# Optimization experiments

Hardware: AMD Instinct MI355X
Metric: run time of the kernel (lower is better)

Reference implementation:

```python
import jax, jax.numpy as jnp
import numpy as np

B, S, D = 8, 4096, 1024
G, V = 2, 320
TAU = 1.0
EPS = 1e-7


def setup_inputs() -> dict:
    key = jax.random.key(0)
    k_x, k_w, k_cb, k_u = jax.random.split(key, 4)
    x = jax.random.normal(k_x, (B, S, D), dtype=jnp.float32)
    W = jax.random.normal(k_w, (D, G * V), dtype=jnp.float32) * (1.0 / np.sqrt(D))
    b = jnp.zeros((G * V,), dtype=jnp.float32)
    # nn.init.uniform_ -> U(0,1); codebooks viewed as [G, V, D//G]
    codebooks = jax.random.uniform(k_cb, (G, V, D // G), dtype=jnp.float32)
    # standard Gumbel(0,1) noise, one per logit: shape [B*S*G, V]
    u = jax.random.uniform(k_u, (B * S * G, V), dtype=jnp.float32,
                           minval=1e-6, maxval=1.0 - 1e-6)
    gumbel = -jnp.log(-jnp.log(u))
    return {"x": x, "W": W, "b": b, "codebooks": codebooks, "gumbel": gumbel}


def reference(x, W, b, codebooks, gumbel):
    Bx, Sx, Dx = x.shape
    Gx, Vx, _ = codebooks.shape
    N = Bx * Sx
    # logit projection: [B,S,D] @ [D, G*V] -> flatten to [N*G, V]
    logits = (jnp.einsum('bsd,de->bse', x, W) + b).reshape(N * Gx, Vx)
    # gumbel-softmax, hard=True with straight-through estimator
    y_soft = jax.nn.softmax((logits + gumbel) / TAU, axis=-1)
    idx = jnp.argmax(y_soft, axis=-1)
    y_hard = jax.nn.one_hot(idx, Vx, dtype=y_soft.dtype)
    one_hot_st = y_hard + y_soft - jax.lax.stop_gradient(y_soft)  # fwd == y_hard
    # codebook lookup via (mostly one-hot) contraction: [N,G,V] x [G,V,d] -> [N,G,d]
    q = jnp.einsum('ngv,gvd->ngd', one_hot_st.reshape(N, Gx, Vx), codebooks)
    quantized = q.reshape(Bx, Sx, Dx)
    # perplexity from clean (non-gumbel) softmax probs
    probs = jax.nn.softmax(logits.reshape(N, Gx, Vx), axis=-1)
    avg_probs = probs.mean(axis=0)  # [G, V]
    perplexity = jnp.exp(-jnp.sum(avg_probs * jnp.log(avg_probs + EPS), axis=-1)).mean()
    return (quantized, perplexity)
```

## Files before the change

kernel.cpp:

```cpp
#include <hip/hip_runtime.h>
#include <math.h>

#define NROWS 32768
#define DD    1024
#define EE    640
#define VV    320
#define BM    128
#define BK    32
#define KT    32
#define CTN   40

typedef __attribute__((ext_vector_type(8))) short short8;
typedef __attribute__((ext_vector_type(4))) short short4v;
typedef __attribute__((ext_vector_type(4))) float float4v;

static __device__ __forceinline__ unsigned short f2bf(float f) {
    unsigned int u = __float_as_uint(f);
    return (unsigned short)((u + 0x7fffu + ((u >> 16) & 1u)) >> 16);
}

static __device__ __forceinline__ void gload_lds16(const void* g, void* l) {
    __builtin_amdgcn_global_load_lds(
        (const __attribute__((address_space(1))) unsigned int*)g,
        (__attribute__((address_space(3))) unsigned int*)l, 16, 0, 0);
}

__global__ void pack_w(const float* __restrict__ W, unsigned short* __restrict__ bp)
{
    const int t = threadIdx.x;
    const int tile = blockIdx.x * 4 + (t >> 6);
    const int lane = t & 63;
    const int kt = tile / CTN, ct = tile % CTN;
    const int k0 = kt * BK + (lane >> 4) * 8;
    const int col = ct * 16 + (lane & 15);
    unsigned short v1[8];
    #pragma unroll
    for (int e = 0; e < 8; ++e)
        v1[e] = f2bf(W[(size_t)(k0 + e) * EE + col]);
    *(short8*)(bp + ((size_t)tile * 64 + lane) * 8) = *(const short8*)v1;
}

__global__ __launch_bounds__(512, 2) void fused_mfma(
    const float* __restrict__ x, const unsigned short* __restrict__ bp,
    const float* __restrict__ bias, const float* __restrict__ cb,
    const float* __restrict__ gum, float* __restrict__ out,
    float* __restrict__ probs_acc)
{
    __shared__ unsigned short Bs[2][BK * EE];
    __shared__ unsigned short As[2][BM * BK];
    __shared__ float probs_blk[EE];
    __shared__ float pmax[4][BM];
    __shared__ float psum[4][BM];
    __shared__ int   pidx[4][BM];
    __shared__ int   fidx[BM][2];
    __shared__ float finv[BM][2];

    const int t    = threadIdx.x;
    const int lane = t & 63;
    const int w    = t >> 6;
    const int rg   = w >> 2;
    const int cg   = w & 3;
    const int n0   = blockIdx.x * BM;

    float4v acc[4][10];
    #pragma unroll
    for (int rf = 0; rf < 4; ++rf)
        #pragma unroll
        for (int ct = 0; ct < 10; ++ct)
            acc[rf][ct] = (float4v)0.f;

    const int row0 = t >> 3, kq0 = t & 7;
    const int abase0 = (row0 >> 4)*512 + ((row0 & 15) + ((kq0 >> 1) << 4))*8 + ((kq0 & 1) << 2);
    const int abase1 = abase0 + 4*512;
    const float* xr0 = x + (size_t)(n0 + row0) * DD + kq0 * 4;
    const float* xr1 = xr0 + (size_t)64 * DD;

    auto writeA = [&](int bb, int base, float4 v) {
        short4v s1;
        s1[0] = (short)f2bf(v.x); s1[1] = (short)f2bf(v.y);
        s1[2] = (short)f2bf(v.z); s1[3] = (short)f2bf(v.w);
        *(short4v*)&As[bb][base] = s1;
    };
    auto stageB = [&](int bb, int kt) {
        const unsigned short* src = bp + (size_t)kt * (BK * EE);
        #pragma unroll
        for (int s = 0; s < 5; ++s) {
            const int q = s * 512 + t;
            gload_lds16(src + (size_t)q * 8, &Bs[bb][q * 8]);
        }
    };

    stageB(0, 0);
    writeA(0, abase0, *(const float4*)(xr0));
    writeA(0, abase1, *(const float4*)(xr1));
    __syncthreads();

    for (int kt = 0; kt < KT; ++kt) {
        const int bb = kt & 1;
        const bool more = (kt + 1 < KT);
        float4 p0, p1;
        if (more) {
            stageB(bb ^ 1, kt + 1);
            p0 = *(const float4*)(xr0 + (kt + 1) * BK);
            p1 = *(const float4*)(xr1 + (kt + 1) * BK);
        }
        short8 af[4];
        #pragma unroll
        for (int rf = 0; rf < 4; ++rf)
            af[rf] = *(const short8*)&As[bb][(rg*4 + rf)*512 + lane*8];
        #pragma unroll
        for (int ct = 0; ct < 10; ++ct) {
            short8 bf = *(const short8*)&Bs[bb][((cg*10 + ct)*64 + lane)*8];
            #pragma unroll
            for (int rf = 0; rf < 4; ++rf)
                acc[rf][ct] = __builtin_amdgcn_mfma_f32_16x16x32_bf16(af[rf], bf, acc[rf][ct], 0, 0, 0);
        }
        if (more) {
            writeA(bb ^ 1, abase0, p0);
            writeA(bb ^ 1, abase1, p1);
        }
        __syncthreads();
    }

    {
        float bv[10];
        #pragma unroll
        for (int ct = 0; ct < 10; ++ct) bv[ct] = bias[cg*160 + ct*16 + (lane & 15)];
        #pragma unroll
        for (int rf = 0; rf < 4; ++rf)
            #pragma unroll
            for (int ct = 0; ct < 10; ++ct) {
                acc[rf][ct][0] += bv[ct]; acc[rf][ct][1] += bv[ct];
                acc[rf][ct][2] += bv[ct]; acc[rf][ct][3] += bv[ct];
            }
    }

    const int g = cg >> 1;
    const int goff0 = (cg & 1)*160 + (lane & 15);
    #pragma unroll
    for (int rf = 0; rf < 4; ++rf) {
        #pragma unroll
        for (int r = 0; r < 4; ++r) {
            const int rowA = rg*64 + rf*16 + ((lane >> 4) << 2) + r;
            const float* grow = gum + ((size_t)(n0 + rowA)*2 + g)*VV + goff0;
            float m1 = -1e30f; int bi = 0; float es = 0.f;
            #pragma unroll
            for (int ct = 0; ct < 10; ++ct) {
                float z  = acc[rf][ct][r];
                float zg = z + grow[ct*16];
                if (zg > m1) { m1 = zg; bi = goff0 + ct*16; }
                es += __expf(z);
            }
            #pragma unroll
            for (int off = 1; off < 16; off <<= 1) {
                float om = __shfl_xor(m1, off);
                int   ob = __shfl_xor(bi, off);
                if (om > m1 || (om == m1 && ob < bi)) { m1 = om; bi = ob; }
                es += __shfl_xor(es, off);
            }
            if ((lane & 15) == 0) {
                pmax[cg][rowA] = m1; pidx[cg][rowA] = bi; psum[cg][rowA] = es;
            }
        }
    }
    __syncthreads();

    if (t < 256) {
        const int row = t & 127, gg = t >> 7;
        const float mA = pmax[gg*2][row], mB = pmax[gg*2+1][row];
        const int   iA = pidx[gg*2][row], iB = pidx[gg*2+1][row];
        fidx[row][gg] = (mB > mA || (mB == mA && iB < iA)) ? iB : iA;
        finv[row][gg] = 1.f / (psum[gg*2][row] + psum[gg*2+1][row]);
    }
    for (int c = t; c < EE; c += 512) probs_blk[c] = 0.f;
    __syncthreads();

    float pacc[10];
    #pragma unroll
    for (int ct = 0; ct < 10; ++ct) pacc[ct] = 0.f;
    #pragma unroll
    for (int rf = 0; rf < 4; ++rf) {
        #pragma unroll
        for (int r = 0; r < 4; ++r) {
            const int rowA = rg*64 + rf*16 + ((lane >> 4) << 2) + r;
            const float inv = finv[rowA][g];
            #pragma unroll
            for (int ct = 0; ct < 10; ++ct)
                pacc[ct] += __expf(acc[rf][ct][r]) * inv;
        }
    }
    #pragma unroll
    for (int off = 16; off < 64; off <<= 1)
        #pragma unroll
        for (int ct = 0; ct < 10; ++ct)
            pacc[ct] += __shfl_xor(pacc[ct], off);
    if (lane < 16) {
        #pragma unroll
        for (int ct = 0; ct < 10; ++ct)
            atomicAdd(&probs_blk[cg*160 + ct*16 + lane], pacc[ct]);
    }
    __syncthreads();

    for (int c = t; c < EE; c += 512)
        atomicAdd(&probs_acc[c], probs_blk[c]);

    for (int i = t; i < BM*256; i += 512) {
        const int row = i >> 8, f4 = i & 255;
        const int gg  = f4 >> 7;
        const int idx = fidx[row][gg];
        const float4 v = *(const float4*)&cb[((size_t)gg*VV + idx)*512 + (size_t)(f4 & 127)*4];
        *(float4*)&out[(size_t)(n0 + row)*DD + (size_t)f4*4] = v;
    }
}

__global__ void perp_kernel(const float* __restrict__ probs_acc,
                            float* __restrict__ outp)
{
    __shared__ float s0[4], s1[4];
    int t = threadIdx.x;
    float p0 = 0.f, p1 = 0.f;
    for (int c = t; c < EE; c += 256) {
        float a = probs_acc[c] * (1.0f / NROWS);
        float v = a * logf(a + 1e-7f);
        if (c < VV) p0 += v; else p1 += v;
    }
    #pragma unroll
    for (int off = 1; off < 64; off <<= 1) {
        p0 += __shfl_xor(p0, off);
        p1 += __shfl_xor(p1, off);
    }
    if ((t & 63) == 0) { s0[t >> 6] = p0; s1[t >> 6] = p1; }
    __syncthreads();
    if (t == 0) {
        float a0 = s0[0] + s0[1] + s0[2] + s0[3];
        float a1 = s1[0] + s1[1] + s1[2] + s1[3];
        outp[0] = 0.5f * (expf(-a0) + expf(-a1));
    }
}

extern "C" void kernel_launch(void* const* d_in, const int* in_sizes, int n_in,
                              void* d_out, int out_size, void* d_ws, size_t ws_size,
                              hipStream_t stream)
{
    const float* x   = (const float*)d_in[0];
    const float* W   = (const float*)d_in[1];
    const float* b   = (const float*)d_in[2];
    const float* cb  = (const float*)d_in[3];
    const float* gum = (const float*)d_in[4];
    float* out = (float*)d_out;

    unsigned short* bp = (unsigned short*)d_ws;
    float* probs_acc = (float*)((char*)d_ws + (size_t)DD*EE*2);

    hipMemsetAsync(probs_acc, 0, EE * sizeof(float), stream);
    pack_w<<<320, 256, 0, stream>>>(W, bp);
    fused_mfma<<<NROWS / BM, 512, 0, stream>>>(x, bp, b, cb, gum, out, probs_acc);
    perp_kernel<<<1, 256, 0, stream>>>(probs_acc, out + (out_size - 1));
}
```

Measured before the change: 135.7 us.

## Drop LDS staging; load A and B fragments directly from global memory

The GEMM kernel now loads x fragments straight from global memory into registers, converts them to bf16 in registers, and reads packed W fragments directly from global memory instead of staging through double-buffered LDS with barriers. The row tile shrinks from 128 to 32 rows and the block from 512 to 256 threads, giving many more blocks and removing every per-k-step __syncthreads. In exchange, each block re-reads the whole packed W from global or L2, so W traffic rises about fourfold, and global-load latency is hidden only by a one-step register prefetch and by occupancy.

```diff
diff --git a/kernel.cpp b/kernel.cpp
--- a/kernel.cpp
+++ b/kernel.cpp
@@ -1,17 +1,16 @@
 #include <hip/hip_runtime.h>
+#include <hip/hip_bf16.h>
 #include <math.h>
 
 #define NROWS 32768
 #define DD    1024
 #define EE    640
 #define VV    320
-#define BM    128
-#define BK    32
+#define BM    32
 #define KT    32
 #define CTN   40
 
 typedef __attribute__((ext_vector_type(8))) short short8;
-typedef __attribute__((ext_vector_type(4))) short short4v;
 typedef __attribute__((ext_vector_type(4))) float float4v;
 
 static __device__ __forceinline__ unsigned short f2bf(float f) {
@@ -19,10 +18,14 @@
     return (unsigned short)((u + 0x7fffu + ((u >> 16) & 1u)) >> 16);
 }
 
-static __device__ __forceinline__ void gload_lds16(const void* g, void* l) {
-    __builtin_amdgcn_global_load_lds(
-        (const __attribute__((address_space(1))) unsigned int*)g,
-        (__attribute__((address_space(3))) unsigned int*)l, 16, 0, 0);
+static __device__ __forceinline__ short8 cvt8(float4 a, float4 b) {
+    float2 f0 = {a.x, a.y}, f1 = {a.z, a.w}, f2 = {b.x, b.y}, f3 = {b.z, b.w};
+    union { __hip_bfloat162 h[4]; short8 s; } u;
+    u.h[0] = __float22bfloat162_rn(f0);
+    u.h[1] = __float22bfloat162_rn(f1);
+    u.h[2] = __float22bfloat162_rn(f2);
+    u.h[3] = __float22bfloat162_rn(f3);
+    return u.s;
 }
 
 __global__ void pack_w(const float* __restrict__ W, unsigned short* __restrict__ bp)
@@ -31,7 +34,7 @@
     const int tile = blockIdx.x * 4 + (t >> 6);
     const int lane = t & 63;
     const int kt = tile / CTN, ct = tile % CTN;
-    const int k0 = kt * BK + (lane >> 4) * 8;
+    const int k0 = kt * 32 + (lane >> 4) * 8;
     const int col = ct * 16 + (lane & 15);
     unsigned short v1[8];
     #pragma unroll
@@ -40,14 +43,12 @@
     *(short8*)(bp + ((size_t)tile * 64 + lane) * 8) = *(const short8*)v1;
 }
 
-__global__ __launch_bounds__(512, 2) void fused_mfma(
+__global__ __launch_bounds__(256, 3) void fused_mfma(
     const float* __restrict__ x, const unsigned short* __restrict__ bp,
     const float* __restrict__ bias, const float* __restrict__ cb,
     const float* __restrict__ gum, float* __restrict__ out,
     float* __restrict__ probs_acc)
 {
-    __shared__ unsigned short Bs[2][BK * EE];
-    __shared__ unsigned short As[2][BM * BK];
     __shared__ float probs_blk[EE];
     __shared__ float pmax[4][BM];
     __shared__ float psum[4][BM];
@@ -57,69 +58,53 @@
 
     const int t    = threadIdx.x;
     const int lane = t & 63;
-    const int w    = t >> 6;
-    const int rg   = w >> 2;
-    const int cg   = w & 3;
+    const int cg   = t >> 6;
     const int n0   = blockIdx.x * BM;
 
-    float4v acc[4][10];
-    #pragma unroll
-    for (int rf = 0; rf < 4; ++rf)
+    float4v acc[2][10];
+    #pragma unroll
+    for (int rf = 0; rf < 2; ++rf)
         #pragma unroll
         for (int ct = 0; ct < 10; ++ct)
             acc[rf][ct] = (float4v)0.f;
 
-    const int row0 = t >> 3, kq0 = t & 7;
-    const int abase0 = (row0 >> 4)*512 + ((row0 & 15) + ((kq0 >> 1) << 4))*8 + ((kq0 & 1) << 2);
-    const int abase1 = abase0 + 4*512;
-    const float* xr0 = x + (size_t)(n0 + row0) * DD + kq0 * 4;
-    const float* xr1 = xr0 + (size_t)64 * DD;
-
-    auto writeA = [&](int bb, int base, float4 v) {
-        short4v s1;
-        s1[0] = (short)f2bf(v.x); s1[1] = (short)f2bf(v.y);
-        s1[2] = (short)f2bf(v.z); s1[3] = (short)f2bf(v.w);
-        *(short4v*)&As[bb][base] = s1;
-    };
-    auto stageB = [&](int bb, int kt) {
-        const unsigned short* src = bp + (size_t)kt * (BK * EE);
-        #pragma unroll
-        for (int s = 0; s < 5; ++s) {
-            const int q = s * 512 + t;
-            gload_lds16(src + (size_t)q * 8, &Bs[bb][q * 8]);
-        }
-    };
-
-    stageB(0, 0);
-    writeA(0, abase0, *(const float4*)(xr0));
-    writeA(0, abase1, *(const float4*)(xr1));
-    __syncthreads();
+    const float* xl = x + (size_t)(n0 + (lane & 15)) * DD + (lane >> 4) * 8;
+    const unsigned short* bpw = bp + ((size_t)cg * 10 * 64 + lane) * 8;
+
+    float4 acur[2][2], anxt[2][2];
+    #pragma unroll
+    for (int rf = 0; rf < 2; ++rf) {
+        acur[rf][0] = *(const float4*)(xl + (size_t)rf * 16 * DD);
+        acur[rf][1] = *(const float4*)(xl + (size_t)rf * 16 * DD + 4);
+    }
 
     for (int kt = 0; kt < KT; ++kt) {
-        const int bb = kt & 1;
-        const bool more = (kt + 1 < KT);
-        float4 p0, p1;
-        if (more) {
-            stageB(bb ^ 1, kt + 1);
-            p0 = *(const float4*)(xr0 + (kt + 1) * BK);
-            p1 = *(const float4*)(xr1 + (kt + 1) * BK);
-        }
-        short8 af[4];
-        #pragma unroll
-        for (int rf = 0; rf < 4; ++rf)
-            af[rf] = *(const short8*)&As[bb][(rg*4 + rf)*512 + lane*8];
+        if (kt + 1 < KT) {
+            const float* xn = xl + (kt + 1) * 32;
+            #pragma unroll
+            for (int rf = 0; rf < 2; ++rf) {
+                anxt[rf][0] = *(const float4*)(xn + (size_t)rf * 16 * DD);
+                anxt[rf][1] = *(const float4*)(xn + (size_t)rf * 16 * DD + 4);
+            }
+        }
+        short8 af[2];
+        #pragma unroll
+        for (int rf = 0; rf < 2; ++rf)
+            af[rf] = cvt8(acur[rf][0], acur[rf][1]);
+
+        const unsigned short* bk = bpw + (size_t)kt * (CTN * 64 * 8);
         #pragma unroll
         for (int ct = 0; ct < 10; ++ct) {
-            short8 bf = *(const short8*)&Bs[bb][((cg*10 + ct)*64 + lane)*8];
-            #pragma unroll
-            for (int rf = 0; rf < 4; ++rf)
+            short8 bf = *(const short8*)(bk + ct * 512);
+            #pragma unroll
+            for (int rf = 0; rf < 2; ++rf)
                 acc[rf][ct] = __builtin_amdgcn_mfma_f32_16x16x32_bf16(af[rf], bf, acc[rf][ct], 0, 0, 0);
         }
-        if (more) {
-            writeA(bb ^ 1, abase0, p0);
-            writeA(bb ^ 1, abase1, p1);
-        }
-        __syncthreads();
+        #pragma unroll
+        for (int rf = 0; rf < 2; ++rf) {
+            acur[rf][0] = anxt[rf][0];
+            acur[rf][1] = anxt[rf][1];
+        }
     }
 
     {
@@ -127,7 +112,7 @@
         #pragma unroll
         for (int ct = 0; ct < 10; ++ct) bv[ct] = bias[cg*160 + ct*16 + (lane & 15)];
         #pragma unroll
-        for (int rf = 0; rf < 4; ++rf)
+        for (int rf = 0; rf < 2; ++rf)
             #pragma unroll
             for (int ct = 0; ct < 10; ++ct) {
                 acc[rf][ct][0] += bv[ct]; acc[rf][ct][1] += bv[ct];
@@ -138,10 +123,10 @@
     const int g = cg >> 1;
     const int goff0 = (cg & 1)*160 + (lane & 15);
     #pragma unroll
-    for (int rf = 0; rf < 4; ++rf) {
+    for (int rf = 0; rf < 2; ++rf) {
         #pragma unroll
         for (int r = 0; r < 4; ++r) {
-            const int rowA = rg*64 + rf*16 + ((lane >> 4) << 2) + r;
+            const int rowA = rf*16 + ((lane >> 4) << 2) + r;
             const float* grow = gum + ((size_t)(n0 + rowA)*2 + g)*VV + goff0;
             float m1 = -1e30f; int bi = 0; float es = 0.f;
             #pragma unroll
@@ -163,26 +148,26 @@
             }
         }
     }
-    __syncthreads();
-
-    if (t < 256) {
-        const int row = t & 127, gg = t >> 7;
+    for (int c = t; c < EE; c += 256) probs_blk[c] = 0.f;
+    __syncthreads();
+
+    if (t < 64) {
+        const int row = t & 31, gg = t >> 5;
         const float mA = pmax[gg*2][row], mB = pmax[gg*2+1][row];
         const int   iA = pidx[gg*2][row], iB = pidx[gg*2+1][row];
         fidx[row][gg] = (mB > mA || (mB == mA && iB < iA)) ? iB : iA;
         finv[row][gg] = 1.f / (psum[gg*2][row] + psum[gg*2+1][row]);
     }
-    for (int c = t; c < EE; c += 512) probs_blk[c] = 0.f;
     __syncthreads();
 
     float pacc[10];
     #pragma unroll
     for (int ct = 0; ct < 10; ++ct) pacc[ct] = 0.f;
     #pragma unroll
-    for (int rf = 0; rf < 4; ++rf) {
+    for (int rf = 0; rf < 2; ++rf) {
         #pragma unroll
         for (int r = 0; r < 4; ++r) {
-            const int rowA = rg*64 + rf*16 + ((lane >> 4) << 2) + r;
+            const int rowA = rf*16 + ((lane >> 4) << 2) + r;
             const float inv = finv[rowA][g];
             #pragma unroll
             for (int ct = 0; ct < 10; ++ct)
@@ -201,15 +186,15 @@
     }
     __syncthreads();
 
-    for (int c = t; c < EE; c += 512)
+    for (int c = t; c < EE; c += 256)
         atomicAdd(&probs_acc[c], probs_blk[c]);
 
-    for (int i = t; i < BM*256; i += 512) {
-        const int row = i >> 8, f4 = i & 255;
-        const int gg  = f4 >> 7;
-        const int idx = fidx[row][gg];
-        const float4 v = *(const float4*)&cb[((size_t)gg*VV + idx)*512 + (size_t)(f4 & 127)*4];
-        *(float4*)&out[(size_t)(n0 + row)*DD + (size_t)f4*4] = v;
+    #pragma unroll 4
+    for (int j = 0; j < BM; ++j) {
+        const int gg  = t >> 7;
+        const int idx = fidx[j][gg];
+        const float4 v = *(const float4*)&cb[((size_t)gg*VV + idx)*512 + (size_t)(t & 127)*4];
+        *(float4*)&out[(size_t)(n0 + j)*DD + (size_t)t*4] = v;
     }
 }
 
@@ -254,6 +239,6 @@
 
     hipMemsetAsync(probs_acc, 0, EE * sizeof(float), stream);
     pack_w<<<320, 256, 0, stream>>>(W, bp);
-    fused_mfma<<<NROWS / BM, 512, 0, stream>>>(x, bp, b, cb, gum, out, probs_acc);
+    fused_mfma<<<NROWS / BM, 256, 0, stream>>>(x, bp, b, cb, gum, out, probs_acc);
     perp_kernel<<<1, 256, 0, stream>>>(probs_acc, out + (out_size - 1));
 }
```

Measured after the change: 278.1 us. +104.9%, slower.

## Halve row tile to 64, single-buffer LDS, raise occupancy to 4 blocks/CU

Applied to the files above, without the earlier changes.

The row tile drops from 128 to 64 and the 8 waves are reorganised so each wave owns all 64 rows and 80 columns, which halves the accumulator registers. LDS double buffering is removed, so each block uses less shared memory, and launch bounds now ask for 4 blocks per CU. The aim is to hide memory latency through more resident blocks rather than in-block prefetch. The cost is an extra barrier per k-step with B staging fully exposed, and each block reloads the whole W slice for half as many rows, doubling total B traffic.

```diff
diff --git a/kernel.cpp b/kernel.cpp
--- a/kernel.cpp
+++ b/kernel.cpp
@@ -1,12 +1,12 @@
 #include <hip/hip_runtime.h>
+#include <hip/hip_bf16.h>
 #include <math.h>
 
 #define NROWS 32768
 #define DD    1024
 #define EE    640
 #define VV    320
-#define BM    128
-#define BK    32
+#define BM    64
 #define KT    32
 #define CTN   40
 
@@ -31,7 +31,7 @@
     const int tile = blockIdx.x * 4 + (t >> 6);
     const int lane = t & 63;
     const int kt = tile / CTN, ct = tile % CTN;
-    const int k0 = kt * BK + (lane >> 4) * 8;
+    const int k0 = kt * 32 + (lane >> 4) * 8;
     const int col = ct * 16 + (lane & 15);
     unsigned short v1[8];
     #pragma unroll
@@ -40,112 +40,105 @@
     *(short8*)(bp + ((size_t)tile * 64 + lane) * 8) = *(const short8*)v1;
 }
 
-__global__ __launch_bounds__(512, 2) void fused_mfma(
+__global__ __launch_bounds__(512, 4) void fused_mfma(
     const float* __restrict__ x, const unsigned short* __restrict__ bp,
     const float* __restrict__ bias, const float* __restrict__ cb,
     const float* __restrict__ gum, float* __restrict__ out,
     float* __restrict__ probs_acc)
 {
-    __shared__ unsigned short Bs[2][BK * EE];
-    __shared__ unsigned short As[2][BM * BK];
+    __shared__ unsigned short Bs[32 * EE];
+    __shared__ unsigned short As[BM * 32];
     __shared__ float probs_blk[EE];
-    __shared__ float pmax[4][BM];
-    __shared__ float psum[4][BM];
-    __shared__ int   pidx[4][BM];
+    __shared__ float pmax[8][BM];
+    __shared__ float psum[8][BM];
+    __shared__ int   pidx[8][BM];
     __shared__ int   fidx[BM][2];
     __shared__ float finv[BM][2];
 
     const int t    = threadIdx.x;
     const int lane = t & 63;
-    const int w    = t >> 6;
-    const int rg   = w >> 2;
-    const int cg   = w & 3;
+    const int cg   = t >> 6;
     const int n0   = blockIdx.x * BM;
 
-    float4v acc[4][10];
+    float4v acc[4][5];
     #pragma unroll
     for (int rf = 0; rf < 4; ++rf)
         #pragma unroll
-        for (int ct = 0; ct < 10; ++ct)
+        for (int ct = 0; ct < 5; ++ct)
             acc[rf][ct] = (float4v)0.f;
 
-    const int row0 = t >> 3, kq0 = t & 7;
-    const int abase0 = (row0 >> 4)*512 + ((row0 & 15) + ((kq0 >> 1) << 4))*8 + ((kq0 & 1) << 2);
-    const int abase1 = abase0 + 4*512;
-    const float* xr0 = x + (size_t)(n0 + row0) * DD + kq0 * 4;
-    const float* xr1 = xr0 + (size_t)64 * DD;
-
-    auto writeA = [&](int bb, int base, float4 v) {
+    const int r0 = t >> 3, kq0 = t & 7;
+    const int abase = (r0 >> 4)*512 + ((r0 & 15) + ((kq0 >> 1) << 4))*8 + ((kq0 & 1) << 2);
+    const float* xr = x + (size_t)(n0 + r0) * DD + kq0 * 4;
+
+    auto writeA = [&](float4 v) {
         short4v s1;
         s1[0] = (short)f2bf(v.x); s1[1] = (short)f2bf(v.y);
         s1[2] = (short)f2bf(v.z); s1[3] = (short)f2bf(v.w);
-        *(short4v*)&As[bb][base] = s1;
+        *(short4v*)&As[abase] = s1;
     };
-    auto stageB = [&](int bb, int kt) {
-        const unsigned short* src = bp + (size_t)kt * (BK * EE);
+    auto stageB = [&](int kt) {
+        const unsigned short* src = bp + (size_t)kt * (32 * EE);
         #pragma unroll
         for (int s = 0; s < 5; ++s) {
             const int q = s * 512 + t;
-            gload_lds16(src + (size_t)q * 8, &Bs[bb][q * 8]);
+            gload_lds16(src + (size_t)q * 8, &Bs[q * 8]);
         }
     };
 
-    stageB(0, 0);
-    writeA(0, abase0, *(const float4*)(xr0));
-    writeA(0, abase1, *(const float4*)(xr1));
+    float4 pA = *(const float4*)(xr);
+    stageB(0);
+    __syncthreads();
+    writeA(pA);
     __syncthreads();
 
     for (int kt = 0; kt < KT; ++kt) {
-        const int bb = kt & 1;
         const bool more = (kt + 1 < KT);
-        float4 p0, p1;
-        if (more) {
-            stageB(bb ^ 1, kt + 1);
-            p0 = *(const float4*)(xr0 + (kt + 1) * BK);
-            p1 = *(const float4*)(xr1 + (kt + 1) * BK);
-        }
+        if (more) pA = *(const float4*)(xr + (kt + 1) * 32);
+
         short8 af[4];
         #pragma unroll
         for (int rf = 0; rf < 4; ++rf)
-            af[rf] = *(const short8*)&As[bb][(rg*4 + rf)*512 + lane*8];
-        #pragma unroll
-        for (int ct = 0; ct < 10; ++ct) {
-            short8 bf = *(const short8*)&Bs[bb][((cg*10 + ct)*64 + lane)*8];
+            af[rf] = *(const short8*)&As[rf*512 + lane*8];
+        #pragma unroll
+        for (int ct = 0; ct < 5; ++ct) {
+            short8 bf = *(const short8*)&Bs[((cg*5 + ct)*64 + lane)*8];
             #pragma unroll
             for (int rf = 0; rf < 4; ++rf)
                 acc[rf][ct] = __builtin_amdgcn_mfma_f32_16x16x32_bf16(af[rf], bf, acc[rf][ct], 0, 0, 0);
         }
+        __syncthreads();
         if (more) {
-            writeA(bb ^ 1, abase0, p0);
-            writeA(bb ^ 1, abase1, p1);
+            stageB(kt + 1);
+            writeA(pA);
         }
         __syncthreads();
     }
 
     {
-        float bv[10];
-        #pragma unroll
-        for (int ct = 0; ct < 10; ++ct) bv[ct] = bias[cg*160 + ct*16 + (lane & 15)];
+        float bv[5];
+        #pragma unroll
+        for (int ct = 0; ct < 5; ++ct) bv[ct] = bias[cg*80 + ct*16 + (lane & 15)];
         #pragma unroll
         for (int rf = 0; rf < 4; ++rf)
             #pragma unroll
-            for (int ct = 0; ct < 10; ++ct) {
+            for (int ct = 0; ct < 5; ++ct) {
                 acc[rf][ct][0] += bv[ct]; acc[rf][ct][1] += bv[ct];
                 acc[rf][ct][2] += bv[ct]; acc[rf][ct][3] += bv[ct];
             }
     }
 
-    const int g = cg >> 1;
-    const int goff0 = (cg & 1)*160 + (lane & 15);
+    const int g = cg >> 2;
+    const int goff0 = (cg & 3)*80 + (lane & 15);
     #pragma unroll
     for (int rf = 0; rf < 4; ++rf) {
         #pragma unroll
         for (int r = 0; r < 4; ++r) {
-            const int rowA = rg*64 + rf*16 + ((lane >> 4) << 2) + r;
+            const int rowA = rf*16 + ((lane >> 4) << 2) + r;
             const float* grow = gum + ((size_t)(n0 + rowA)*2 + g)*VV + goff0;
             float m1 = -1e30f; int bi = 0; float es = 0.f;
             #pragma unroll
-            for (int ct = 0; ct < 10; ++ct) {
+            for (int ct = 0; ct < 5; ++ct) {
                 float z  = acc[rf][ct][r];
                 float zg = z + grow[ct*16];
                 if (zg > m1) { m1 = zg; bi = goff0 + ct*16; }
@@ -163,41 +156,47 @@
             }
         }
     }
-    __syncthreads();
-
-    if (t < 256) {
-        const int row = t & 127, gg = t >> 7;
-        const float mA = pmax[gg*2][row], mB = pmax[gg*2+1][row];
-        const int   iA = pidx[gg*2][row], iB = pidx[gg*2+1][row];
-        fidx[row][gg] = (mB > mA || (mB == mA && iB < iA)) ? iB : iA;
-        finv[row][gg] = 1.f / (psum[gg*2][row] + psum[gg*2+1][row]);
-    }
     for (int c = t; c < EE; c += 512) probs_blk[c] = 0.f;
     __syncthreads();
 
-    float pacc[10];
-    #pragma unroll
-    for (int ct = 0; ct < 10; ++ct) pacc[ct] = 0.f;
+    if (t < 128) {
+        const int row = t & 63, gg = t >> 6;
+        float m1 = -1e30f; int bi = 0x7fffffff; float s = 0.f;
+        #pragma unroll
+        for (int c = 0; c < 4; ++c) {
+            const float om = pmax[gg*4 + c][row];
+            const int   ob = pidx[gg*4 + c][row];
+            if (om > m1 || (om == m1 && ob < bi)) { m1 = om; bi = ob; }
+            s += psum[gg*4 + c][row];
+        }
+        fidx[row][gg] = bi;
+        finv[row][gg] = 1.f / s;
+    }
+    __syncthreads();
+
+    float pacc[5];
+    #pragma unroll
+    for (int ct = 0; ct < 5; ++ct) pacc[ct] = 0.f;
     #pragma unroll
     for (int rf = 0; rf < 4; ++rf) {
         #pragma unroll
         for (int r = 0; r < 4; ++r) {
-            const int rowA = rg*64 + rf*16 + ((lane >> 4) << 2) + r;
+            const int rowA = rf*16 + ((lane >> 4) << 2) + r;
             const float inv = finv[rowA][g];
             #pragma unroll
-            for (int ct = 0; ct < 10; ++ct)
+            for (int ct = 0; ct < 5; ++ct)
                 pacc[ct] += __expf(acc[rf][ct][r]) * inv;
         }
     }
     #pragma unroll
     for (int off = 16; off < 64; off <<= 1)
         #pragma unroll
-        for (int ct = 0; ct < 10; ++ct)
+        for (int ct = 0; ct < 5; ++ct)
             pacc[ct] += __shfl_xor(pacc[ct], off);
     if (lane < 16) {
         #pragma unroll
-        for (int ct = 0; ct < 10; ++ct)
-            atomicAdd(&probs_blk[cg*160 + ct*16 + lane], pacc[ct]);
+        for (int ct = 0; ct < 5; ++ct)
+            atomicAdd(&probs_blk[cg*80 + ct*16 + lane], pacc[ct]);
     }
     __syncthreads();
 
```

Result: faster. 131.0 us (-3.5%).

## Read packed W fragments directly from global and replicate probability accumulators

Applied to the files above, without the earlier changes.

Removes the LDS double-buffer for the packed bf16 weight matrix, so each wave loads its B fragments straight from global memory (L2-resident) instead of staging them through shared memory with global_load_lds. This cuts LDS usage substantially, which may allow more blocks per CU, but adds global-load latency to the MFMA inner loop that is no longer hidden by asynchronous staging. Probability atomics are also spread across 8 replicated accumulators to reduce contention, and the final kernel sums the replicas.

```diff
diff --git a/kernel.cpp b/kernel.cpp
--- a/kernel.cpp
+++ b/kernel.cpp
@@ -1,4 +1,5 @@
 #include <hip/hip_runtime.h>
+#include <hip/hip_bf16.h>
 #include <math.h>
 
 #define NROWS 32768
@@ -6,7 +7,6 @@
 #define EE    640
 #define VV    320
 #define BM    128
-#define BK    32
 #define KT    32
 #define CTN   40
 
@@ -17,12 +17,6 @@
 static __device__ __forceinline__ unsigned short f2bf(float f) {
     unsigned int u = __float_as_uint(f);
     return (unsigned short)((u + 0x7fffu + ((u >> 16) & 1u)) >> 16);
-}
-
-static __device__ __forceinline__ void gload_lds16(const void* g, void* l) {
-    __builtin_amdgcn_global_load_lds(
-        (const __attribute__((address_space(1))) unsigned int*)g,
-        (__attribute__((address_space(3))) unsigned int*)l, 16, 0, 0);
 }
 
 __global__ void pack_w(const float* __restrict__ W, unsigned short* __restrict__ bp)
@@ -31,7 +25,7 @@
     const int tile = blockIdx.x * 4 + (t >> 6);
     const int lane = t & 63;
     const int kt = tile / CTN, ct = tile % CTN;
-    const int k0 = kt * BK + (lane >> 4) * 8;
+    const int k0 = kt * 32 + (lane >> 4) * 8;
     const int col = ct * 16 + (lane & 15);
     unsigned short v1[8];
     #pragma unroll
@@ -40,14 +34,13 @@
     *(short8*)(bp + ((size_t)tile * 64 + lane) * 8) = *(const short8*)v1;
 }
 
-__global__ __launch_bounds__(512, 2) void fused_mfma(
+__global__ __launch_bounds__(512, 2) void fused_vq(
     const float* __restrict__ x, const unsigned short* __restrict__ bp,
     const float* __restrict__ bias, const float* __restrict__ cb,
     const float* __restrict__ gum, float* __restrict__ out,
-    float* __restrict__ probs_acc)
-{
-    __shared__ unsigned short Bs[2][BK * EE];
-    __shared__ unsigned short As[2][BM * BK];
+    float* __restrict__ probs_rep)
+{
+    __shared__ unsigned short As[2][BM * 32];
     __shared__ float probs_blk[EE];
     __shared__ float pmax[4][BM];
     __shared__ float psum[4][BM];
@@ -69,28 +62,19 @@
         for (int ct = 0; ct < 10; ++ct)
             acc[rf][ct] = (float4v)0.f;
 
-    const int row0 = t >> 3, kq0 = t & 7;
-    const int abase0 = (row0 >> 4)*512 + ((row0 & 15) + ((kq0 >> 1) << 4))*8 + ((kq0 & 1) << 2);
+    const int r0 = t >> 3, kq0 = t & 7;
+    const int abase0 = (r0 >> 4)*512 + ((r0 & 15) + ((kq0 >> 1) << 4))*8 + ((kq0 & 1) << 2);
     const int abase1 = abase0 + 4*512;
-    const float* xr0 = x + (size_t)(n0 + row0) * DD + kq0 * 4;
+    const float* xr0 = x + (size_t)(n0 + r0) * DD + kq0 * 4;
     const float* xr1 = xr0 + (size_t)64 * DD;
 
     auto writeA = [&](int bb, int base, float4 v) {
-        short4v s1;
-        s1[0] = (short)f2bf(v.x); s1[1] = (short)f2bf(v.y);
-        s1[2] = (short)f2bf(v.z); s1[3] = (short)f2bf(v.w);
-        *(short4v*)&As[bb][base] = s1;
+        short4v s;
+        s[0] = (short)f2bf(v.x); s[1] = (short)f2bf(v.y);
+        s[2] = (short)f2bf(v.z); s[3] = (short)f2bf(v.w);
+        *(short4v*)&As[bb][base] = s;
     };
-    auto stageB = [&](int bb, int kt) {
-        const unsigned short* src = bp + (size_t)kt * (BK * EE);
-        #pragma unroll
-        for (int s = 0; s < 5; ++s) {
-            const int q = s * 512 + t;
-            gload_lds16(src + (size_t)q * 8, &Bs[bb][q * 8]);
-        }
-    };
-
-    stageB(0, 0);
+
     writeA(0, abase0, *(const float4*)(xr0));
     writeA(0, abase1, *(const float4*)(xr1));
     __syncthreads();
@@ -100,17 +84,18 @@
         const bool more = (kt + 1 < KT);
         float4 p0, p1;
         if (more) {
-            stageB(bb ^ 1, kt + 1);
-            p0 = *(const float4*)(xr0 + (kt + 1) * BK);
-            p1 = *(const float4*)(xr1 + (kt + 1) * BK);
+            p0 = *(const float4*)(xr0 + (kt + 1) * 32);
+            p1 = *(const float4*)(xr1 + (kt + 1) * 32);
         }
         short8 af[4];
         #pragma unroll
         for (int rf = 0; rf < 4; ++rf)
             af[rf] = *(const short8*)&As[bb][(rg*4 + rf)*512 + lane*8];
+
+        const unsigned short* fb = bp + (((size_t)kt*CTN + cg*10)*64 + lane)*8;
         #pragma unroll
         for (int ct = 0; ct < 10; ++ct) {
-            short8 bf = *(const short8*)&Bs[bb][((cg*10 + ct)*64 + lane)*8];
+            short8 bf = *(const short8*)(fb + ct*512);
             #pragma unroll
             for (int rf = 0; rf < 4; ++rf)
                 acc[rf][ct] = __builtin_amdgcn_mfma_f32_16x16x32_bf16(af[rf], bf, acc[rf][ct], 0, 0, 0);
@@ -163,6 +148,7 @@
             }
         }
     }
+    for (int c = t; c < EE; c += 512) probs_blk[c] = 0.f;
     __syncthreads();
 
     if (t < 256) {
@@ -172,7 +158,6 @@
         fidx[row][gg] = (mB > mA || (mB == mA && iB < iA)) ? iB : iA;
         finv[row][gg] = 1.f / (psum[gg*2][row] + psum[gg*2+1][row]);
     }
-    for (int c = t; c < EE; c += 512) probs_blk[c] = 0.f;
     __syncthreads();
 
     float pacc[10];
@@ -201,8 +186,9 @@
     }
     __syncthreads();
 
+    const int rep = blockIdx.x & 7;
     for (int c = t; c < EE; c += 512)
-        atomicAdd(&probs_acc[c], probs_blk[c]);
+        atomicAdd(&probs_rep[rep*EE + c], probs_blk[c]);
 
     for (int i = t; i < BM*256; i += 512) {
         const int row = i >> 8, f4 = i & 255;
@@ -213,14 +199,17 @@
     }
 }
 
-__global__ void perp_kernel(const float* __restrict__ probs_acc,
-                            float* __restrict__ outp)
+__global__ void perp8_kernel(const float* __restrict__ probs_rep,
+                             float* __restrict__ outp)
 {
     __shared__ float s0[4], s1[4];
     int t = threadIdx.x;
     float p0 = 0.f, p1 = 0.f;
     for (int c = t; c < EE; c += 256) {
-        float a = probs_acc[c] * (1.0f / NROWS);
+        float a = 0.f;
+        #pragma unroll
+        for (int rp = 0; rp < 8; ++rp) a += probs_rep[rp*EE + c];
+        a *= (1.0f / NROWS);
         float v = a * logf(a + 1e-7f);
         if (c < VV) p0 += v; else p1 += v;
     }
@@ -249,11 +238,14 @@
     const float* gum = (const float*)d_in[4];
     float* out = (float*)d_out;
 
-    unsigned short* bp = (unsigned short*)d_ws;
-    float* probs_acc = (float*)((char*)d_ws + (size_t)DD*EE*2);
-
-    hipMemsetAsync(probs_acc, 0, EE * sizeof(float), stream);
+    char* wsp = (char*)d_ws;
+    unsigned short* bp = (unsigned short*)wsp;
+    const size_t bp_b = (size_t)DD*EE*2;
+    float* probs_rep = (float*)(wsp + bp_b);
+    const size_t pr_b = 8*EE*sizeof(float);
+
+    hipMemsetAsync(probs_rep, 0, pr_b, stream);
     pack_w<<<320, 256, 0, stream>>>(W, bp);
-    fused_mfma<<<NROWS / BM, 512, 0, stream>>>(x, bp, b, cb, gum, out, probs_acc);
-    perp_kernel<<<1, 256, 0, stream>>>(probs_acc, out + (out_size - 1));
-}
+    fused_vq<<<NROWS / BM, 512, 0, stream>>>(x, bp, b, cb, gum, out, probs_rep);
+    perp8_kernel<<<1, 256, 0, stream>>>(probs_rep, out + (out_size - 1));
+}
```

Result: slower. 150.9 us (+11.2%).
